# Performance work log

Hardware: AMD Instinct MI355X
Metric: run time of the kernel (lower is better)

Reference implementation:

```python
import jax, jax.numpy as jnp
import numpy as np

B, S, D, H = 2, 2048, 1024, 16
HD = D // H  # head_dim = 64


def setup_inputs() -> dict:
    key = jax.random.key(0)
    ks = jax.random.split(key, 5)
    scale = 0.02
    return {
        "x": jax.random.normal(ks[0], (B, S, D), dtype=jnp.float32),
        "q_w": jax.random.normal(ks[1], (D, D), dtype=jnp.float32) * scale,
        "k_w": jax.random.normal(ks[2], (D, D), dtype=jnp.float32) * scale,
        "v_w": jax.random.normal(ks[3], (D, D), dtype=jnp.float32) * scale,
        "o_w": jax.random.normal(ks[4], (D, D), dtype=jnp.float32) * scale,
    }


def _mhsa(x, q_w, k_w, v_w, o_w):
    b, s, d = x.shape
    # projections: weight is [out, in] as in torch Parameter usage
    Q = jnp.einsum('bsd,kd->bsk', x, q_w)
    K = jnp.einsum('bsd,kd->bsk', x, k_w)
    V = jnp.einsum('bsd,kd->bsk', x, v_w)
    # split heads: b s (h hd) -> b h s hd
    Q = Q.reshape(b, s, H, HD).transpose(0, 2, 1, 3)
    K = K.reshape(b, s, H, HD).transpose(0, 2, 1, 3)
    V = V.reshape(b, s, H, HD).transpose(0, 2, 1, 3)
    scores = jnp.einsum('bhqd,bhkd->bhqk', Q, K) / jnp.sqrt(jnp.float32(HD))
    causal = jnp.tril(jnp.ones((s, s), dtype=bool))  # [s, s]
    neg_inf = jnp.finfo(scores.dtype).min
    scores = jnp.where(causal[None, None], scores, neg_inf)
    attn = jax.nn.softmax(scores, axis=-1)
    O = jnp.einsum('bhqk,bhkd->bhqd', attn, V)
    O = O.transpose(0, 2, 1, 3).reshape(b, s, d)  # b h s hd -> b s (h hd)
    return jnp.einsum('bsv,dv->bsd', O, o_w)


def reference(x, q_w, k_w, v_w, o_w):
    return _mhsa(x, q_w, k_w, v_w, o_w)
```

## Files before the change

kernel.cpp:

```cpp
#include <hip/hip_runtime.h>


typedef __bf16 bf16x8 __attribute__((ext_vector_type(8)));
typedef float f32x4 __attribute__((ext_vector_type(4)));
typedef float f32x16 __attribute__((ext_vector_type(16)));

#define AS1 __attribute__((address_space(1)))
#define AS3 __attribute__((address_space(3)))

__device__ __forceinline__ ushort f2bf(float f) {
  unsigned u = __builtin_bit_cast(unsigned, f);
  u += 0x7fffu + ((u >> 16) & 1u);
  return (ushort)(u >> 16);
}

__device__ __forceinline__ unsigned cvt_pk_bf16(float lo, float hi) {
  unsigned r;
  asm("v_cvt_pk_bf16_f32 %0, %1, %2" : "=v"(r) : "v"(lo), "v"(hi));
  return r;
}

__device__ __forceinline__ bf16x8 ld16(const ushort* p) {
  return __builtin_bit_cast(bf16x8, *(const uint4*)p);
}

__device__ __forceinline__ void gload16(const ushort* g, ushort* l) {
  __builtin_amdgcn_global_load_lds((const AS1 void*)g, (AS3 void*)l, 16, 0, 0);
}

#define MFMA32(a, b, c) __builtin_amdgcn_mfma_f32_32x32x16_bf16(a, b, c, 0, 0, 0)

__global__ void cast_all(const float4* __restrict__ x, const float4* __restrict__ qw,
                         const float4* __restrict__ kw, const float4* __restrict__ vw,
                         const float4* __restrict__ ow, ushort4* __restrict__ out) {
  const int nx = 1 << 20;
  const int nw = 1 << 18;
  int stride = gridDim.x * blockDim.x;
  for (int i = blockIdx.x * blockDim.x + threadIdx.x; i < nx + 4 * nw; i += stride) {
    const float4* s;
    int off;
    if (i < nx) { s = x; off = i; }
    else {
      int j = i - nx, seg = j >> 18;
      off = j & (nw - 1);
      s = seg == 0 ? qw : seg == 1 ? kw : seg == 2 ? vw : ow;
    }
    float4 v = s[off];
    ushort4 r;
    r.x = f2bf(v.x); r.y = f2bf(v.y); r.z = f2bf(v.z); r.w = f2bf(v.w);
    out[i] = r;
  }
}

template <bool F32OUT>
__device__ __forceinline__ void gemm_body(const ushort* __restrict__ A,
                                          const ushort* __restrict__ B,
                                          void* __restrict__ Cv,
                                          int bm, int bn, int N, int K,
                                          ushort* As, ushort* Bs) {
  const int tid = threadIdx.x;
  const int lane = tid & 63;
  const int wave = tid >> 6;
  const int r15 = lane & 15, hi = lane >> 4;
  const int wm = (wave >> 1) * 64, wn = (wave & 1) * 64;

  f32x4 acc[4][4] = {};

  const int KT = K >> 6;
  for (int kt = 0; kt < KT; ++kt) {
#pragma unroll
    for (int i = 0; i < 4; ++i) {
      int c = i * 256 + tid;
      int row = c >> 3, slot = c & 7;
      int coff = kt * 64 + ((((slot * 16) ^ ((row & 7) << 4))) >> 1);
      gload16(A + (size_t)(bm + row) * K + coff, As + c * 8);
      gload16(B + (size_t)(bn + row) * K + coff, Bs + c * 8);
    }
    __syncthreads();
#pragma unroll
    for (int kc = 0; kc < 2; ++kc) {
      bf16x8 af[4], bfr[4];
#pragma unroll
      for (int mi = 0; mi < 4; ++mi) {
        int ra = wm + mi * 16 + r15;
        af[mi] = ld16(As + ra * 64 + ((kc * 32 + hi * 8) ^ ((ra & 7) << 3)));
      }
#pragma unroll
      for (int nj = 0; nj < 4; ++nj) {
        int rb = wn + nj * 16 + r15;
        bfr[nj] = ld16(Bs + rb * 64 + ((kc * 32 + hi * 8) ^ ((rb & 7) << 3)));
      }
#pragma unroll
      for (int mi = 0; mi < 4; ++mi)
#pragma unroll
        for (int nj = 0; nj < 4; ++nj)
          acc[mi][nj] = __builtin_amdgcn_mfma_f32_16x16x32_bf16(af[mi], bfr[nj], acc[mi][nj], 0, 0, 0);
    }
    __syncthreads();
  }

#pragma unroll
  for (int mi = 0; mi < 4; ++mi)
#pragma unroll
    for (int nj = 0; nj < 4; ++nj) {
      int row = bm + wm + mi * 16 + hi * 4;
      int col = bn + wn + nj * 16 + r15;
#pragma unroll
      for (int j = 0; j < 4; ++j) {
        if (F32OUT)
          ((float*)Cv)[(size_t)(row + j) * N + col] = acc[mi][nj][j];
        else
          ((ushort*)Cv)[(size_t)(row + j) * N + col] = f2bf(acc[mi][nj][j]);
      }
    }
}

template <bool F32OUT>
__global__ __launch_bounds__(256) void gemm_nt(const ushort* __restrict__ A,
                                               const ushort* __restrict__ B,
                                               void* __restrict__ Cv,
                                               int M, int N, int K) {
  __shared__ ushort As[128 * 64];
  __shared__ ushort Bs[128 * 64];
  gemm_body<F32OUT>(A, B, Cv, blockIdx.y * 128, blockIdx.x * 128, N, K, As, Bs);
}

__global__ __launch_bounds__(256) void gemm_qkvt(const ushort* __restrict__ xb,
                                                 const ushort* __restrict__ wqk,
                                                 const ushort* __restrict__ wv,
                                                 ushort* __restrict__ QKb,
                                                 ushort* __restrict__ VT) {
  __shared__ ushort As[128 * 64];
  __shared__ ushort Bs[128 * 64];
  if (blockIdx.x < 16)
    gemm_body<false>(xb, wqk, QKb, blockIdx.y * 128, blockIdx.x * 128, 2048, 1024, As, Bs);
  else
    gemm_body<false>(wv, xb, VT, (blockIdx.x - 16) * 128, blockIdx.y * 128, 4096, 1024, As, Bs);
}

__global__ __launch_bounds__(512, 4) void attn_fwd(const ushort* __restrict__ QK,
                                                   const ushort* __restrict__ VT,
                                                   ushort* __restrict__ Ob) {
  __shared__ __align__(16) ushort lds[33024];
  ushort* Ks0 = lds;
  ushort* Vs0 = lds + 16384;
  float* mlsh = (float*)(lds + 32768);
  float* osh = (float*)lds;

  const int tid = threadIdx.x, lane = tid & 63, wave = tid >> 6;
  const int l31 = lane & 31, hi = lane >> 5;
  const int kh = wave >> 2;
  const int hw = wave & 3;
  const int bh = blockIdx.x;
  const int y = blockIdx.y;
  const int qt = (y & 8) ? (15 - (y & 7)) : (y & 7);
  const int nh = 2 * (qt + 1);
  const size_t base = (size_t)(bh >> 4) * (2048 * 2048) + (bh & 15) * 64;
  const int qbase = qt * 128 + hw * 32;
  const int qrow = qbase + l31;
  const size_t KSTEP = (size_t)32 * 2048;

  bf16x8 qf[4];
  {
    const ushort* qp = QK + base + (size_t)qrow * 2048 + hi * 8;
#pragma unroll
    for (int c = 0; c < 4; ++c) qf[c] = ld16(qp + c * 16);
  }

  const int krow = tid >> 3, kslot = tid & 7;
  const int ksub = krow >> 5;
  const ushort* kg = QK + base + 1024 +
                     (size_t)((ksub * nh) * 32 + (krow & 31)) * 2048 +
                     ((((kslot * 16) ^ ((krow & 7) << 4))) >> 1);
  const int vd = tid >> 3;
  const int slotx = (tid & 7) ^ (vd & 7);
  const ushort* vgp = VT + (size_t)((bh & 15) * 64 + vd) * 4096 + (bh >> 4) * 2048 +
                      (size_t)((slotx >> 2) * nh) * 32 + (slotx & 3) * 8;

  f32x16 o0 = {}, o1 = {};
  float l_r = 0.f;
  const float Cc = 0.125f * 1.44269504f;

  {
    gload16(kg, Ks0 + tid * 8);
    gload16(vgp, Vs0 + tid * 8);
    gload16(kg + KSTEP, Ks0 + 4096 + tid * 8);
    gload16(vgp + 32, Vs0 + 4096 + tid * 8);
  }
  __syncthreads();

  for (int tt = 0; tt < nh; tt += 2) {
    const int pb = (tt >> 1) & 1;
    if (tt + 2 < nh) {
      gload16(kg + (size_t)(tt + 2) * KSTEP, Ks0 + (pb ^ 1) * 8192 + tid * 8);
      gload16(vgp + (size_t)(tt + 2) * 32, Vs0 + (pb ^ 1) * 8192 + tid * 8);
      gload16(kg + (size_t)(tt + 3) * KSTEP, Ks0 + (pb ^ 1) * 8192 + 4096 + tid * 8);
      gload16(vgp + (size_t)(tt + 3) * 32, Vs0 + (pb ^ 1) * 8192 + 4096 + tid * 8);
    }

#pragma unroll
    for (int u = 0; u < 2; ++u) {
      const int t = tt + u;
      const ushort* Kb = Ks0 + pb * 8192 + u * 4096;
      const ushort* Vb = Vs0 + pb * 8192 + u * 4096;
      const int kvb = (kh * nh + t) * 32;
      if (kvb <= qbase + 31) {
        f32x16 s = {};
        __builtin_amdgcn_s_setprio(1);
#pragma unroll
        for (int c = 0; c < 4; ++c) {
          int col = c * 16 + hi * 8;
          int r0 = kh * 32 + l31;
          bf16x8 k0 = ld16(Kb + r0 * 64 + (col ^ ((r0 & 7) << 3)));
          s = MFMA32(k0, qf[c], s);
        }
        __builtin_amdgcn_s_setprio(0);

        if (kvb + 31 > qbase) {
#pragma unroll
          for (int r = 0; r < 16; ++r) {
            int kvl = (r & 3) + 8 * (r >> 2) + 4 * hi;
            if (kvb + kvl > qrow) s[r] = -3e38f;
          }
        }

        float p[16];
#pragma unroll
        for (int r = 0; r < 16; ++r) p[r] = exp2f(s[r] * Cc);
        float ts[8];
#pragma unroll
        for (int r = 0; r < 8; ++r) ts[r] = p[r] + p[r + 8];
#pragma unroll
        for (int off = 4; off > 0; off >>= 1)
#pragma unroll
          for (int r = 0; r < off; ++r) ts[r] += ts[r + off];
        l_r += ts[0] + __shfl_xor(ts[0], 32);

#pragma unroll
        for (int c = 0; c < 2; ++c) {
          const int o = c * 8;
          unsigned uA0 = cvt_pk_bf16(p[o + 0], p[o + 1]);
          unsigned uA1 = cvt_pk_bf16(p[o + 2], p[o + 3]);
          unsigned uB0 = cvt_pk_bf16(p[o + 4], p[o + 5]);
          unsigned uB1 = cvt_pk_bf16(p[o + 6], p[o + 7]);
          unsigned r0x = __shfl_xor(hi ? uA0 : uB0, 32);
          unsigned r1x = __shfl_xor(hi ? uA1 : uB1, 32);
          uint4 y4;
          y4.x = hi ? r0x : uA0;
          y4.y = hi ? r1x : uA1;
          y4.z = hi ? uB0 : r0x;
          y4.w = hi ? uB1 : r1x;
          bf16x8 pf = __builtin_bit_cast(bf16x8, y4);

          int col = kh * 32 + c * 16 + hi * 8;
          int d0r = l31, d1r = 32 + l31;
          bf16x8 v0 = ld16(Vb + d0r * 64 + (col ^ ((d0r & 7) << 3)));
          bf16x8 v1 = ld16(Vb + d1r * 64 + (col ^ ((d1r & 7) << 3)));
          __builtin_amdgcn_s_setprio(1);
          o0 = MFMA32(v0, pf, o0);
          o1 = MFMA32(v1, pf, o1);
          __builtin_amdgcn_s_setprio(0);
        }
      }
    }

    __syncthreads();
  }

  if (kh) {
#pragma unroll
    for (int r = 0; r < 16; ++r) {
      osh[(hw * 32 + r) * 64 + lane] = o0[r];
      osh[(hw * 32 + 16 + r) * 64 + lane] = o1[r];
    }
    if (lane < 32) mlsh[hw * 32 + lane] = l_r;
  }
  __syncthreads();
  if (!kh) {
    float l_hi = mlsh[hw * 32 + l31];
    float lm = l_r + l_hi;
    float linv = lm > 0.f ? 1.0f / lm : 0.f;
#pragma unroll
    for (int r = 0; r < 16; ++r) {
      o0[r] = (o0[r] + osh[(hw * 32 + r) * 64 + lane]) * linv;
      o1[r] = (o1[r] + osh[(hw * 32 + 16 + r) * 64 + lane]) * linv;
    }
  }
  __syncthreads();
  if (!kh) {
    ushort* sm = lds;
    int q = hw * 32 + l31;
#pragma unroll
    for (int r = 0; r < 16; ++r) {
      int d = (r & 3) + 8 * (r >> 2) + 4 * hi;
      sm[q * 64 + (d ^ ((q & 7) << 3))] = f2bf(o0[r]);
      int d2 = d + 32;
      sm[q * 64 + (d2 ^ ((q & 7) << 3))] = f2bf(o1[r]);
    }
  }
  __syncthreads();
#pragma unroll
  for (int i = 0; i < 2; ++i) {
    int idx = i * 512 + tid;
    int row = idx >> 3, slot = idx & 7;
    uint4 v = *(const uint4*)(lds + row * 64 + ((slot * 8) ^ ((row & 7) << 3)));
    *(uint4*)(Ob + ((size_t)((bh >> 4) * 2048 + qt * 128 + row)) * 1024 +
              (bh & 15) * 64 + slot * 8) = v;
  }
}

extern "C" void kernel_launch(void* const* d_in, const int* in_sizes, int n_in,
                              void* d_out, int out_size, void* d_ws, size_t ws_size,
                              hipStream_t stream) {
  (void)in_sizes; (void)n_in; (void)out_size; (void)ws_size;
  const float* x = (const float*)d_in[0];
  const float* qw = (const float*)d_in[1];
  const float* kw = (const float*)d_in[2];
  const float* vw = (const float*)d_in[3];
  const float* ow = (const float*)d_in[4];
  float* out = (float*)d_out;

  const int NT = 4096;
  const int D = 1024;

  ushort* xb    = (ushort*)d_ws;
  ushort* wqkv  = xb + (size_t)NT * D;
  ushort* wob   = wqkv + (size_t)3 * D * D;
  ushort* QKb   = wob + (size_t)D * D;
  ushort* VT    = QKb + (size_t)NT * 2 * D;
  ushort* Ob    = VT + (size_t)D * NT;

  cast_all<<<2048, 256, 0, stream>>>((const float4*)x, (const float4*)qw,
                                     (const float4*)kw, (const float4*)vw,
                                     (const float4*)ow, (ushort4*)xb);

  gemm_qkvt<<<dim3(24, 32), 256, 0, stream>>>(xb, wqkv, wqkv + (size_t)2 * D * D, QKb, VT);

  attn_fwd<<<dim3(32, 16), 512, 0, stream>>>(QKb, VT, Ob);

  gemm_nt<true><<<dim3(D / 128, NT / 128), 256, 0, stream>>>(Ob, wob, out, NT, D, D);
}
```

Before: 102.0 us.

## Split attention blocks into 64-row halves, pair q-tiles, and four-way KV split

Each attention block now handles a 64-row half of a query tile. It processes two paired q-tiles (jq and 15-jq) in sequence, which balances the causal work across blocks. The 8 waves are reorganised from 2 KV-halves × 4 q-groups into 4 KV-quarters × 2 q-groups, with a four-way reduction of partial O and l through LDS. The V tile layout widens to 128 columns per row to hold the quarter streams. This adds extra syncs and reduction traffic, and one KV tile is loaded per iteration instead of two.

```diff
diff --git a/kernel.cpp b/kernel.cpp
--- a/kernel.cpp
+++ b/kernel.cpp
@@ -141,68 +141,73 @@
 __global__ __launch_bounds__(512, 4) void attn_fwd(const ushort* __restrict__ QK,
                                                    const ushort* __restrict__ VT,
                                                    ushort* __restrict__ Ob) {
-  __shared__ __align__(16) ushort lds[33024];
+  __shared__ __align__(16) ushort lds[33152];
   ushort* Ks0 = lds;
   ushort* Vs0 = lds + 16384;
   float* mlsh = (float*)(lds + 32768);
   float* osh = (float*)lds;
+  ushort* sm = lds + 24576;
 
   const int tid = threadIdx.x, lane = tid & 63, wave = tid >> 6;
   const int l31 = lane & 31, hi = lane >> 5;
-  const int kh = wave >> 2;
-  const int hw = wave & 3;
+  const int kh = wave >> 1;
+  const int hw = wave & 1;
   const int bh = blockIdx.x;
-  const int y = blockIdx.y;
-  const int qt = (y & 8) ? (15 - (y & 7)) : (y & 7);
-  const int nh = 2 * (qt + 1);
+  const int jq = blockIdx.y & 7, half = blockIdx.y >> 3;
   const size_t base = (size_t)(bh >> 4) * (2048 * 2048) + (bh & 15) * 64;
-  const int qbase = qt * 128 + hw * 32;
-  const int qrow = qbase + l31;
   const size_t KSTEP = (size_t)32 * 2048;
 
-  bf16x8 qf[4];
-  {
-    const ushort* qp = QK + base + (size_t)qrow * 2048 + hi * 8;
-#pragma unroll
-    for (int c = 0; c < 4; ++c) qf[c] = ld16(qp + c * 16);
-  }
-
-  const int krow = tid >> 3, kslot = tid & 7;
-  const int ksub = krow >> 5;
-  const ushort* kg = QK + base + 1024 +
-                     (size_t)((ksub * nh) * 32 + (krow & 31)) * 2048 +
-                     ((((kslot * 16) ^ ((krow & 7) << 4))) >> 1);
-  const int vd = tid >> 3;
-  const int slotx = (tid & 7) ^ (vd & 7);
-  const ushort* vgp = VT + (size_t)((bh & 15) * 64 + vd) * 4096 + (bh >> 4) * 2048 +
-                      (size_t)((slotx >> 2) * nh) * 32 + (slotx & 3) * 8;
-
-  f32x16 o0 = {}, o1 = {};
-  float l_r = 0.f;
+  const int krow = tid >> 3;
+  const int kcol = ((((tid & 7) * 16) ^ ((krow & 7) << 4)) >> 1);
+  const int ks0 = krow >> 5;
+  const int vd0 = tid >> 4;
+  const int sgx = (tid & 15) ^ (vd0 & 7);
+  const int vstream = sgx >> 2;
+  const int vkv = (sgx & 3) * 8;
+
   const float Cc = 0.125f * 1.44269504f;
 
-  {
-    gload16(kg, Ks0 + tid * 8);
-    gload16(vgp, Vs0 + tid * 8);
-    gload16(kg + KSTEP, Ks0 + 4096 + tid * 8);
-    gload16(vgp + 32, Vs0 + 4096 + tid * 8);
-  }
-  __syncthreads();
-
-  for (int tt = 0; tt < nh; tt += 2) {
-    const int pb = (tt >> 1) & 1;
-    if (tt + 2 < nh) {
-      gload16(kg + (size_t)(tt + 2) * KSTEP, Ks0 + (pb ^ 1) * 8192 + tid * 8);
-      gload16(vgp + (size_t)(tt + 2) * 32, Vs0 + (pb ^ 1) * 8192 + tid * 8);
-      gload16(kg + (size_t)(tt + 3) * KSTEP, Ks0 + (pb ^ 1) * 8192 + 4096 + tid * 8);
-      gload16(vgp + (size_t)(tt + 3) * 32, Vs0 + (pb ^ 1) * 8192 + 4096 + tid * 8);
-    }
-
-#pragma unroll
-    for (int u = 0; u < 2; ++u) {
-      const int t = tt + u;
-      const ushort* Kb = Ks0 + pb * 8192 + u * 4096;
-      const ushort* Vb = Vs0 + pb * 8192 + u * 4096;
+#pragma unroll 1
+  for (int ph = 0; ph < 2; ++ph) {
+    const int qtp = ph ? (15 - jq) : jq;
+    const int nh = qtp + 1;
+    const int qbase = qtp * 128 + half * 64 + hw * 32;
+    const int qrow = qbase + l31;
+
+    const ushort* kgp = QK + base + 1024 + (size_t)(krow & 31) * 2048 + kcol;
+    const ushort* kg0 = kgp + (size_t)(ks0 * nh) * KSTEP;
+    const ushort* kg1 = kgp + (size_t)((2 + ks0) * nh) * KSTEP;
+    const ushort* vg0 = VT + (size_t)((bh & 15) * 64 + vd0) * 4096 +
+                        (bh >> 4) * 2048 + (size_t)(vstream * nh) * 32 + vkv;
+    const ushort* vg1 = vg0 + (size_t)32 * 4096;
+
+    bf16x8 qf[4];
+    {
+      const ushort* qp = QK + base + (size_t)qrow * 2048 + hi * 8;
+#pragma unroll
+      for (int c = 0; c < 4; ++c) qf[c] = ld16(qp + c * 16);
+    }
+
+    f32x16 o0 = {}, o1 = {};
+    float l_r = 0.f;
+
+    gload16(kg0, Ks0 + tid * 8);
+    gload16(kg1, Ks0 + (512 + tid) * 8);
+    gload16(vg0, Vs0 + tid * 8);
+    gload16(vg1, Vs0 + (512 + tid) * 8);
+    __syncthreads();
+
+    for (int t = 0; t < nh; ++t) {
+      const int buf = t & 1;
+      if (t + 1 < nh) {
+        gload16(kg0 + (size_t)(t + 1) * KSTEP, Ks0 + (buf ^ 1) * 8192 + tid * 8);
+        gload16(kg1 + (size_t)(t + 1) * KSTEP, Ks0 + (buf ^ 1) * 8192 + (512 + tid) * 8);
+        gload16(vg0 + (size_t)(t + 1) * 32, Vs0 + (buf ^ 1) * 8192 + tid * 8);
+        gload16(vg1 + (size_t)(t + 1) * 32, Vs0 + (buf ^ 1) * 8192 + (512 + tid) * 8);
+      }
+
+      const ushort* Kb = Ks0 + buf * 8192;
+      const ushort* Vb = Vs0 + buf * 8192;
       const int kvb = (kh * nh + t) * 32;
       if (kvb <= qbase + 31) {
         f32x16 s = {};
@@ -254,58 +259,54 @@
 
           int col = kh * 32 + c * 16 + hi * 8;
           int d0r = l31, d1r = 32 + l31;
-          bf16x8 v0 = ld16(Vb + d0r * 64 + (col ^ ((d0r & 7) << 3)));
-          bf16x8 v1 = ld16(Vb + d1r * 64 + (col ^ ((d1r & 7) << 3)));
+          bf16x8 v0 = ld16(Vb + d0r * 128 + (col ^ ((d0r & 7) << 3)));
+          bf16x8 v1 = ld16(Vb + d1r * 128 + (col ^ ((d1r & 7) << 3)));
           __builtin_amdgcn_s_setprio(1);
           o0 = MFMA32(v0, pf, o0);
           o1 = MFMA32(v1, pf, o1);
           __builtin_amdgcn_s_setprio(0);
         }
       }
-    }
-
-    __syncthreads();
-  }
-
-  if (kh) {
-#pragma unroll
-    for (int r = 0; r < 16; ++r) {
-      osh[(hw * 32 + r) * 64 + lane] = o0[r];
-      osh[(hw * 32 + 16 + r) * 64 + lane] = o1[r];
-    }
-    if (lane < 32) mlsh[hw * 32 + lane] = l_r;
-  }
-  __syncthreads();
-  if (!kh) {
-    float l_hi = mlsh[hw * 32 + l31];
-    float lm = l_r + l_hi;
-    float linv = lm > 0.f ? 1.0f / lm : 0.f;
-#pragma unroll
-    for (int r = 0; r < 16; ++r) {
-      o0[r] = (o0[r] + osh[(hw * 32 + r) * 64 + lane]) * linv;
-      o1[r] = (o1[r] + osh[(hw * 32 + 16 + r) * 64 + lane]) * linv;
-    }
-  }
-  __syncthreads();
-  if (!kh) {
-    ushort* sm = lds;
-    int q = hw * 32 + l31;
-#pragma unroll
-    for (int r = 0; r < 16; ++r) {
-      int d = (r & 3) + 8 * (r >> 2) + 4 * hi;
-      sm[q * 64 + (d ^ ((q & 7) << 3))] = f2bf(o0[r]);
-      int d2 = d + 32;
-      sm[q * 64 + (d2 ^ ((q & 7) << 3))] = f2bf(o1[r]);
-    }
-  }
-  __syncthreads();
-#pragma unroll
-  for (int i = 0; i < 2; ++i) {
-    int idx = i * 512 + tid;
-    int row = idx >> 3, slot = idx & 7;
-    uint4 v = *(const uint4*)(lds + row * 64 + ((slot * 8) ^ ((row & 7) << 3)));
-    *(uint4*)(Ob + ((size_t)((bh >> 4) * 2048 + qt * 128 + row)) * 1024 +
-              (bh & 15) * 64 + slot * 8) = v;
+
+      __syncthreads();
+    }
+
+    if (kh) {
+#pragma unroll
+      for (int r = 0; r < 16; ++r) {
+        osh[((kh - 1) * 64 + hw * 32 + r) * 64 + lane] = o0[r];
+        osh[((kh - 1) * 64 + hw * 32 + 16 + r) * 64 + lane] = o1[r];
+      }
+      if (lane < 32) mlsh[(kh - 1) * 64 + hw * 32 + l31] = l_r;
+    }
+    __syncthreads();
+    if (!kh) {
+      float lm = l_r + mlsh[hw * 32 + l31] + mlsh[64 + hw * 32 + l31] +
+                 mlsh[128 + hw * 32 + l31];
+      float linv = lm > 0.f ? 1.0f / lm : 0.f;
+      int q = hw * 32 + l31;
+#pragma unroll
+      for (int r = 0; r < 16; ++r) {
+        float v0 = (o0[r] + osh[(hw * 32 + r) * 64 + lane] +
+                    osh[(64 + hw * 32 + r) * 64 + lane] +
+                    osh[(128 + hw * 32 + r) * 64 + lane]) * linv;
+        float v1 = (o1[r] + osh[(hw * 32 + 16 + r) * 64 + lane] +
+                    osh[(64 + hw * 32 + 16 + r) * 64 + lane] +
+                    osh[(128 + hw * 32 + 16 + r) * 64 + lane]) * linv;
+        int d = (r & 3) + 8 * (r >> 2) + 4 * hi;
+        sm[q * 64 + (d ^ ((q & 7) << 3))] = f2bf(v0);
+        int d2 = d + 32;
+        sm[q * 64 + (d2 ^ ((q & 7) << 3))] = f2bf(v1);
+      }
+    }
+    __syncthreads();
+    {
+      int row = tid >> 3, slot = tid & 7;
+      uint4 v = *(const uint4*)(sm + row * 64 + ((slot * 8) ^ ((row & 7) << 3)));
+      *(uint4*)(Ob + ((size_t)((bh >> 4) * 2048 + qtp * 128 + half * 64 + row)) * 1024 +
+                (bh & 15) * 64 + slot * 8) = v;
+    }
+    __syncthreads();
   }
 }
 
```

New measurement: 117.7 us. 15.3% more time.
